# Kernel tuning notes

Hardware: AMD Instinct MI355X
Metric: run time of the kernel (lower is better)

## Reference

```python
import jax, jax.numpy as jnp
import numpy as np

B, DIM, HEADS, Hs, Ws = 8, 192, 8, 128, 128


def setup_inputs() -> dict:
    key = jax.random.key(0)
    ks = jax.random.split(key, 8)
    d3 = 3 * DIM
    inp = {
        "x": jax.random.normal(ks[0], (B, DIM, Hs, Ws), dtype=jnp.float32),
        # qkv 1x1 conv: (out=3*dim, in=dim)
        "w_qkv": jax.random.normal(ks[1], (d3, DIM), dtype=jnp.float32) / np.sqrt(DIM),
        "b_qkv": jnp.zeros((d3,), dtype=jnp.float32),
        # depthwise 3x3 conv, groups = 3*dim -> kernel (3*dim, 1, 3, 3)
        "w_dw": jax.random.normal(ks[2], (d3, 1, 3, 3), dtype=jnp.float32) / 3.0,
        "b_dw": jnp.zeros((d3,), dtype=jnp.float32),
        # project_out 1x1 conv: (dim, dim)
        "w_proj": jax.random.normal(ks[3], (DIM, DIM), dtype=jnp.float32) / np.sqrt(DIM),
        "b_proj": jnp.zeros((DIM,), dtype=jnp.float32),
        "temperature": jnp.ones((HEADS, 1, 1), dtype=jnp.float32),
        "a1": jnp.full((1,), 0.2, dtype=jnp.float32),
        "a2": jnp.full((1,), 0.2, dtype=jnp.float32),
        "a3": jnp.full((1,), 0.2, dtype=jnp.float32),
        "a4": jnp.full((1,), 0.2, dtype=jnp.float32),
    }
    return inp


def _sparse_softmax(attn, k):
    # top-k per row, scatter 1s at those indices, mask rest to -inf, softmax
    _, idx = jax.lax.top_k(attn, k)                      # [..., C, k]
    C = attn.shape[-1]
    mask = jax.nn.one_hot(idx, C, dtype=attn.dtype).sum(-2)  # [..., C, C]
    masked = jnp.where(mask > 0, attn, -jnp.inf)
    return jax.nn.softmax(masked, axis=-1)


def _l2norm(t):
    # torch F.normalize: x / max(||x||_2, eps) along last axis
    n = jnp.sqrt(jnp.sum(t * t, axis=-1, keepdims=True))
    return t / jnp.maximum(n, 1e-12)


def reference(x, w_qkv, b_qkv, w_dw, b_dw, w_proj, b_proj, temperature, a1, a2, a3, a4):
    b, c, h, w = x.shape
    # 1x1 conv
    qkv = jnp.einsum('oi,bihw->bohw', w_qkv, x) + b_qkv[:, None, None]
    # depthwise 3x3 conv, padding=1
    qkv = jax.lax.conv_general_dilated(
        qkv, w_dw, window_strides=(1, 1), padding='SAME',
        feature_group_count=3 * c,
        dimension_numbers=('NCHW', 'OIHW', 'NCHW')) + b_dw[:, None, None]
    q, k, v = jnp.split(qkv, 3, axis=1)
    Cd = c // HEADS  # per-head channel dim
    heads = lambda t: t.reshape(b, HEADS, Cd, h * w)
    q, k, v = heads(q), heads(k), heads(v)
    q, k = _l2norm(q), _l2norm(k)
    # transposed (channel) attention: [b, head, Cd, Cd]
    attn = jnp.einsum('bhcn,bhdn->bhcd', q, k) * temperature
    ks = (int(Cd / 2), int(Cd * 2 / 3), int(Cd * 3 / 4), int(Cd * 4 / 5))
    out1 = jnp.einsum('bhcd,bhdn->bhcn', _sparse_softmax(attn, ks[0]), v)
    out2 = jnp.einsum('bhcd,bhdn->bhcn', _sparse_softmax(attn, ks[1]), v)
    out3 = jnp.einsum('bhcd,bhdn->bhcn', _sparse_softmax(attn, ks[2]), v)
    out4 = jnp.einsum('bhcd,bhdn->bhcn', _sparse_softmax(attn, ks[3]), v)
    out = out1 * a1 + out2 * a2 + out3 * a3 + out4 * a4
    out = out.reshape(b, c, h, w)
    out = jnp.einsum('oi,bihw->bohw', w_proj, out) + b_proj[:, None, None]
    return out
```

## Files before the change

### kernel.cpp

```cpp
#include <hip/hip_runtime.h>
#include <math.h>

#define DIMC 192
#define C3 576
#define NHEADS 8
#define CDh 24
#define HWN 16384
#define WIDTH 128
#define NBATCH 8

typedef __attribute__((ext_vector_type(8))) short short8;
typedef __attribute__((ext_vector_type(4))) float f32x4;

__device__ __forceinline__ ushort f2bf(float f) {
    uint u = __float_as_uint(f);
    u += 0x7fff + ((u >> 16) & 1);
    return (ushort)(u >> 16);
}
__device__ __forceinline__ float bf2f(ushort h) {
    return __uint_as_float(((uint)h) << 16);
}

__global__ void k0_prep(const float* __restrict__ W, ushort* __restrict__ Wh,
                        ushort* __restrict__ Wl, int n) {
    int i = blockIdx.x * 256 + threadIdx.x;
    if (i < n) {
        float w = W[i];
        ushort h = f2bf(w);
        Wh[i] = h;
        Wl[i] = f2bf(w - bf2f(h));
    }
}

__global__ __launch_bounds__(256, 3) void kgx3(const float* __restrict__ x,
                                               const ushort* __restrict__ Wh,
                                               const ushort* __restrict__ Wl,
                                               const float* __restrict__ bias,
                                               float* __restrict__ qkv, long qkv_zs) {
    __shared__ ushort smem[2 * 64 * 200];
    ushort* BsH = smem;
    ushort* BsL = smem + 64 * 200;
    const float* xb = x + (size_t)blockIdx.z * DIMC * HWN;
    float* oz = qkv + (size_t)blockIdx.z * qkv_zs;
    const int n0 = blockIdx.x * 64;
    const int o0 = blockIdx.y * 192;
    const int tid = threadIdx.x;
#pragma unroll
    for (int it = 0; it < 12; it++) {
        int idx = tid + it * 256;
        int ch = idx >> 4, q = idx & 15;
        f32x4 v = *(const f32x4*)&xb[(size_t)ch * HWN + n0 + q * 4];
        const int swz = ((ch >> 3) ^ (q & 7)) * 8 + (ch & 7);
#pragma unroll
        for (int p = 0; p < 4; p++) {
            int ad = (q * 4 + p) * 200 + swz;
            ushort hb = f2bf(v[p]);
            BsH[ad] = hb;
            BsL[ad] = f2bf(v[p] - bf2f(hb));
        }
    }
    __syncthreads();
    const int wid = tid >> 6, lane = tid & 63;
    const int lr = lane & 15, lk = lane >> 4;
    const int mb = o0 + wid * 48;
    f32x4 acc[3][4];
#pragma unroll
    for (int i = 0; i < 3; i++)
#pragma unroll
        for (int j = 0; j < 4; j++) acc[i][j] = (f32x4)0.f;

    for (int kc6 = 0; kc6 < 6; kc6++) {
        short8 bh[4], bl[4];
#pragma unroll
        for (int j = 0; j < 4; j++) {
            int px = j * 16 + lr;
            int o = (kc6 * 4 + lk) ^ ((px >> 2) & 7);
            int ad = px * 200 + o * 8;
            bh[j] = *(const short8*)&BsH[ad];
            bl[j] = *(const short8*)&BsL[ad];
        }
#pragma unroll
        for (int i = 0; i < 3; i++) {
            size_t ao = (size_t)(mb + i * 16 + lr) * DIMC + kc6 * 32 + lk * 8;
            const short8 ah = *(const short8*)&Wh[ao];
            const short8 al = *(const short8*)&Wl[ao];
#pragma unroll
            for (int j = 0; j < 4; j++) {
                acc[i][j] = __builtin_amdgcn_mfma_f32_16x16x32_bf16(ah, bh[j], acc[i][j], 0, 0, 0);
                acc[i][j] = __builtin_amdgcn_mfma_f32_16x16x32_bf16(ah, bl[j], acc[i][j], 0, 0, 0);
                acc[i][j] = __builtin_amdgcn_mfma_f32_16x16x32_bf16(al, bh[j], acc[i][j], 0, 0, 0);
            }
        }
    }
    __syncthreads();
    float* epsb = (float*)smem + wid * (2 * 1056);
#pragma unroll
    for (int i = 0; i < 3; i++) {
        float* eps = epsb + (i & 1) * 1056;
        int rb = mb + i * 16;
#pragma unroll
        for (int j = 0; j < 4; j++)
#pragma unroll
            for (int r = 0; r < 4; r++)
                eps[(lk * 4 + r) * 66 + j * 16 + lr] = acc[i][j][r] + bias[rb + lk * 4 + r];
#pragma unroll
        for (int s = 0; s < 4; s++) {
            int rl = s * 4 + (lane >> 4);
            int c4 = (lane & 15) * 4;
            f32x4 v = *(const f32x4*)&eps[rl * 66 + c4];
            *(f32x4*)&oz[(size_t)(rb + rl) * HWN + n0 + c4] = v;
        }
    }
}

__global__ __launch_bounds__(256, 3) void kg3f(float* __restrict__ vy,
                                               const ushort* __restrict__ Mh,
                                               const ushort* __restrict__ Ml,
                                               const float* __restrict__ bias) {
    __shared__ ushort smem[2 * 64 * 200];
    ushort* BsH = smem;
    ushort* BsL = smem + 64 * 200;
    const int z = blockIdx.y;
    float* vb = vy + (size_t)z * DIMC * HWN;
    const int n0 = blockIdx.x * 64;
    const int tid = threadIdx.x;
#pragma unroll
    for (int it = 0; it < 12; it++) {
        int idx = tid + it * 256;
        int ch = idx >> 4, q = idx & 15;
        f32x4 v = *(const f32x4*)&vb[(size_t)ch * HWN + n0 + q * 4];
        const int swz = ((ch >> 3) ^ (q & 7)) * 8 + (ch & 7);
#pragma unroll
        for (int p = 0; p < 4; p++) {
            int ad = (q * 4 + p) * 200 + swz;
            ushort hb = f2bf(v[p]);
            BsH[ad] = hb;
            BsL[ad] = f2bf(v[p] - bf2f(hb));
        }
    }
    __syncthreads();
    const int wid = tid >> 6, lane = tid & 63;
    const int lr = lane & 15, lk = lane >> 4;
    const int mb = wid * 48;
    const ushort* Azh = Mh + (size_t)z * DIMC * DIMC;
    const ushort* Azl = Ml + (size_t)z * DIMC * DIMC;
    f32x4 acc[3][4];
#pragma unroll
    for (int i = 0; i < 3; i++)
#pragma unroll
        for (int j = 0; j < 4; j++) acc[i][j] = (f32x4)0.f;

    for (int kc6 = 0; kc6 < 6; kc6++) {
        short8 bh[4], bl[4];
#pragma unroll
        for (int j = 0; j < 4; j++) {
            int px = j * 16 + lr;
            int o = (kc6 * 4 + lk) ^ ((px >> 2) & 7);
            int ad = px * 200 + o * 8;
            bh[j] = *(const short8*)&BsH[ad];
            bl[j] = *(const short8*)&BsL[ad];
        }
#pragma unroll
        for (int i = 0; i < 3; i++) {
            size_t ao = (size_t)(mb + i * 16 + lr) * DIMC + kc6 * 32 + lk * 8;
            const short8 ah = *(const short8*)&Azh[ao];
            const short8 al = *(const short8*)&Azl[ao];
#pragma unroll
            for (int j = 0; j < 4; j++) {
                acc[i][j] = __builtin_amdgcn_mfma_f32_16x16x32_bf16(ah, bh[j], acc[i][j], 0, 0, 0);
                acc[i][j] = __builtin_amdgcn_mfma_f32_16x16x32_bf16(ah, bl[j], acc[i][j], 0, 0, 0);
                acc[i][j] = __builtin_amdgcn_mfma_f32_16x16x32_bf16(al, bh[j], acc[i][j], 0, 0, 0);
            }
        }
    }
    __syncthreads();
    float* epsb = (float*)smem + wid * (2 * 1056);
#pragma unroll
    for (int i = 0; i < 3; i++) {
        float* eps = epsb + (i & 1) * 1056;
        int rb = mb + i * 16;
#pragma unroll
        for (int j = 0; j < 4; j++)
#pragma unroll
            for (int r = 0; r < 4; r++)
                eps[(lk * 4 + r) * 66 + j * 16 + lr] = acc[i][j][r] + bias[rb + lk * 4 + r];
#pragma unroll
        for (int s = 0; s < 4; s++) {
            int rl = s * 4 + (lane >> 4);
            int c4 = (lane & 15) * 4;
            f32x4 v = *(const f32x4*)&eps[rl * 66 + c4];
            *(f32x4*)&vb[(size_t)(rb + rl) * HWN + n0 + c4] = v;
        }
    }
}

__global__ __launch_bounds__(1024, 4) void k2_dw(const float* __restrict__ qkv0, long qkv_zs,
                                                 const float* __restrict__ wdw,
                                                 const float* __restrict__ bdw,
                                                 float* __restrict__ vout,
                                                 float* __restrict__ part, int b0) {
    __shared__ float stage[2 * 6336];
    __shared__ float qks[48 * 520];
    const int b = b0 + blockIdx.z;
    const float* qkv = qkv0 + (size_t)blockIdx.z * qkv_zs;
    const int stripe = blockIdx.x, h = blockIdx.y;
    const int tid = threadIdx.x;
    const int r0 = stripe * 4;

    const int col4 = (tid & 31) * 4;
    const int orow = (tid >> 5) & 3;
    const int cc = tid >> 7;

    auto stage_load = [&](int chunk, int buf) {
        const int g = chunk / 3, cb = (chunk % 3) * 8;
        float* sb = stage + buf * 6336;
#pragma unroll
        for (int f = tid; f < 1536; f += 1024) {
            int fc = f / 192, rem = f - fc * 192;
            int rl = rem >> 5, c4 = rem & 31;
            int gr = r0 - 1 + rl;
            int ch = g * DIMC + h * CDh + cb + fc;
            float4 v = make_float4(0.f, 0.f, 0.f, 0.f);
            if (gr >= 0 && gr < 128)
                v = *(const float4*)&qkv[(size_t)ch * HWN + gr * WIDTH + c4 * 4];
            *(float4*)&sb[(fc * 6 + rl) * 132 + c4 * 4] = v;
        }
    };

    stage_load(0, 0);
    __syncthreads();
    for (int chunk = 0; chunk < 9; chunk++) {
        const int buf = chunk & 1;
        if (chunk < 8) stage_load(chunk + 1, buf ^ 1);
        const int g = chunk / 3, cb = (chunk % 3) * 8;
        const float* sb = stage + buf * 6336;
        const int ch = g * DIMC + h * CDh + cb + cc;
        float wr[9];
#pragma unroll
        for (int t = 0; t < 9; t++) wr[t] = wdw[ch * 9 + t];
        float bsv = bdw[ch];
        float a0 = bsv, a1 = bsv, a2 = bsv, a3 = bsv;
#pragma unroll
        for (int dr = 0; dr < 3; dr++) {
            const float* row = &sb[(cc * 6 + orow + dr) * 132];
            f32x4 cen = *(const f32x4*)&row[col4];
            f32x4 lf4 = (col4 > 0) ? *(const f32x4*)&row[col4 - 4] : (f32x4)0.f;
            f32x4 rt4 = (col4 < 124) ? *(const f32x4*)&row[col4 + 4] : (f32x4)0.f;
            float left = lf4[3], right = rt4[0];
            float wA = wr[dr * 3 + 0], wB = wr[dr * 3 + 1], wC = wr[dr * 3 + 2];
            a0 = fmaf(left, wA, fmaf(cen[0], wB, fmaf(cen[1], wC, a0)));
            a1 = fmaf(cen[0], wA, fmaf(cen[1], wB, fmaf(cen[2], wC, a1)));
            a2 = fmaf(cen[1], wA, fmaf(cen[2], wB, fmaf(cen[3], wC, a2)));
            a3 = fmaf(cen[2], wA, fmaf(cen[3], wB, fmaf(right, wC, a3)));
        }
        if (g < 2) {
            float4 o4 = {a0, a1, a2, a3};
            *(float4*)&qks[(g * CDh + cb + cc) * 520 + orow * 128 + col4] = o4;
        } else {
            float4 o4 = {a0, a1, a2, a3};
            *(float4*)&vout[((size_t)b * DIMC + h * CDh + cb + cc) * HWN +
                            (size_t)(r0 + orow) * WIDTH + col4] = o4;
        }
        __syncthreads();
    }

    const int tc = tid & 3, td = (tid >> 2) & 3, tp = tid >> 4;
    float ga[6][6];
#pragma unroll
    for (int i = 0; i < 6; i++)
#pragma unroll
        for (int j = 0; j < 6; j++) ga[i][j] = 0.f;
#pragma unroll
    for (int s = 0; s < 2; s++) {
        int px = tp * 8 + s * 4;
        f32x4 qv[6], kv[6];
#pragma unroll
        for (int i = 0; i < 6; i++) qv[i] = *(const f32x4*)&qks[(tc * 6 + i) * 520 + px];
#pragma unroll
        for (int j = 0; j < 6; j++) kv[j] = *(const f32x4*)&qks[(24 + td * 6 + j) * 520 + px];
#pragma unroll
        for (int i = 0; i < 6; i++)
#pragma unroll
            for (int j = 0; j < 6; j++) {
                ga[i][j] = fmaf(qv[i][0], kv[j][0], ga[i][j]);
                ga[i][j] = fmaf(qv[i][1], kv[j][1], ga[i][j]);
                ga[i][j] = fmaf(qv[i][2], kv[j][2], ga[i][j]);
                ga[i][j] = fmaf(qv[i][3], kv[j][3], ga[i][j]);
            }
    }
#pragma unroll
    for (int i = 0; i < 6; i++)
#pragma unroll
        for (int j = 0; j < 6; j++) {
            float v = ga[i][j];
            v += __shfl_xor(v, 16, 64);
            v += __shfl_xor(v, 32, 64);
            ga[i][j] = v;
        }
    float nv = 0.f;
    int nch = 0, npg = 0;
    if (tid < 768) {
        npg = tid / 48;
        nch = tid - npg * 48;
#pragma unroll
        for (int s = 0; s < 8; s++) {
            f32x4 v = *(const f32x4*)&qks[nch * 520 + npg * 32 + s * 4];
            nv = fmaf(v[0], v[0], nv);
            nv = fmaf(v[1], v[1], nv);
            nv = fmaf(v[2], v[2], nv);
            nv = fmaf(v[3], v[3], nv);
        }
    }
    __syncthreads();
    float* gscr = qks;
    const int wave = tid >> 6;
    if ((tid & 63) < 16) {
#pragma unroll
        for (int i = 0; i < 6; i++)
#pragma unroll
            for (int j = 0; j < 6; j++)
                gscr[wave * 624 + (tc * 6 + i) * 24 + (td * 6 + j)] = ga[i][j];
    }
    if (tid < 768) gscr[npg * 624 + 576 + nch] = nv;
    __syncthreads();
    if (tid < 624) {
        float s = 0.f;
#pragma unroll
        for (int w2 = 0; w2 < 16; w2++) s += gscr[w2 * 624 + tid];
        part[((size_t)(b * NHEADS + h) * 64 + stripe) * 624 + tid] = s;
    }
}

__global__ void k34_attn(const float* __restrict__ part, const float* __restrict__ temp,
                         const float* __restrict__ a1, const float* __restrict__ a2,
                         const float* __restrict__ a3, const float* __restrict__ a4,
                         float* __restrict__ Aeff) {
    __shared__ float gbuf[624];
    int bh = blockIdx.x;
    int h = bh & 7;
    int tid = threadIdx.x;
    for (int ti = tid; ti < 624; ti += 256) {
        float s = 0.f;
        const float* p = part + (size_t)bh * 64 * 624 + ti;
#pragma unroll 4
        for (int st = 0; st < 32; st++) s += p[st * 624];
        gbuf[ti] = s;
    }
    __syncthreads();
    int r = tid;
    if (r >= CDh) return;
    float t = temp[h];
    float aw[4] = {a1[0], a2[0], a3[0], a4[0]};
    const int kks[4] = {12, 16, 18, 19};
    float qn = fmaxf(sqrtf(gbuf[576 + r]), 1e-12f);
    float av[24];
    for (int d = 0; d < 24; d++) {
        float kn = fmaxf(sqrtf(gbuf[600 + d]), 1e-12f);
        av[d] = gbuf[r * 24 + d] / (qn * kn) * t;
    }
    int rank[24];
    float m = -1e30f;
    for (int d = 0; d < 24; d++) {
        int rk = 0;
        for (int e = 0; e < 24; e++)
            rk += (av[e] > av[d]) || (av[e] == av[d] && e < d);
        rank[d] = rk;
        m = fmaxf(m, av[d]);
    }
    float ex[24], outv[24];
    for (int d = 0; d < 24; d++) { ex[d] = expf(av[d] - m); outv[d] = 0.f; }
    for (int i = 0; i < 4; i++) {
        float Z = 0.f;
        for (int d = 0; d < 24; d++) if (rank[d] < kks[i]) Z += ex[d];
        float inv = aw[i] / Z;
        for (int d = 0; d < 24; d++) if (rank[d] < kks[i]) outv[d] += ex[d] * inv;
    }
    for (int d = 0; d < 24; d++) Aeff[(bh * 24 + r) * 24 + d] = outv[d];
}

__global__ void k4b_mmat(const float* __restrict__ Wp, const float* __restrict__ Aeff,
                         ushort* __restrict__ Mh, ushort* __restrict__ Ml) {
    int b = blockIdx.x;
    int e0 = blockIdx.y * 6144;
    for (int e = e0 + threadIdx.x; e < e0 + 6144; e += 256) {
        int o = e / DIMC, j = e % DIMC;
        int h = j / CDh, d = j % CDh;
        const float* wrow = Wp + o * DIMC + h * CDh;
        const float* acol = Aeff + (size_t)((b * NHEADS + h) * CDh) * CDh + d;
        float s = 0.f;
        for (int c = 0; c < CDh; c++) s = fmaf(wrow[c], acol[c * CDh], s);
        size_t idx = ((size_t)b * DIMC + o) * DIMC + j;
        ushort hb = f2bf(s);
        Mh[idx] = hb;
        Ml[idx] = f2bf(s - bf2f(hb));
    }
}

extern "C" void kernel_launch(void* const* d_in, const int* in_sizes, int n_in,
                              void* d_out, int out_size, void* d_ws, size_t ws_size,
                              hipStream_t stream) {
    const float* x     = (const float*)d_in[0];
    const float* wqkv  = (const float*)d_in[1];
    const float* bqkv  = (const float*)d_in[2];
    const float* wdw   = (const float*)d_in[3];
    const float* bdw   = (const float*)d_in[4];
    const float* wproj = (const float*)d_in[5];
    const float* bproj = (const float*)d_in[6];
    const float* temp  = (const float*)d_in[7];
    const float* a1    = (const float*)d_in[8];
    const float* a2    = (const float*)d_in[9];
    const float* a3    = (const float*)d_in[10];
    const float* a4    = (const float*)d_in[11];
    float* out = (float*)d_out;

    float* ws = (float*)d_ws;
    const size_t fl_part = (size_t)64 * 64 * 624;
    const size_t fl_A    = (size_t)64 * 576;
    const size_t fl_M    = (size_t)NBATCH * DIMC * DIMC / 2;
    const size_t fl_W    = (size_t)C3 * DIMC / 2;
    const size_t fl_qkv1 = (size_t)C3 * HWN;
    const size_t base_fl = fl_part + fl_A + 2 * fl_M + 2 * fl_W;

    int nz = (ws_size >= (base_fl + 2 * fl_qkv1) * sizeof(float)) ? 2 : 1;

    size_t o = 0;
    float* part = ws + o; o += fl_part;
    float* Aeff = ws + o; o += fl_A;
    ushort* Mh  = (ushort*)(ws + o); o += fl_M;
    ushort* Ml  = (ushort*)(ws + o); o += fl_M;
    ushort* Wh  = (ushort*)(ws + o); o += fl_W;
    ushort* Wl  = (ushort*)(ws + o); o += fl_W;
    float* qkv  = ws + o;

    const long qkv_zs = (long)fl_qkv1;

    k0_prep<<<(C3 * DIMC + 255) / 256, 256, 0, stream>>>(wqkv, Wh, Wl, C3 * DIMC);

    for (int b0 = 0; b0 < NBATCH; b0 += nz) {
        kgx3<<<dim3(256, 3, nz), 256, 0, stream>>>(x + (size_t)b0 * DIMC * HWN,
                                                   Wh, Wl, bqkv, qkv, qkv_zs);
        k2_dw<<<dim3(32, 8, nz), 1024, 0, stream>>>(qkv, qkv_zs, wdw, bdw, out, part, b0);
    }
    k34_attn<<<64, 256, 0, stream>>>(part, temp, a1, a2, a3, a4, Aeff);
    k4b_mmat<<<dim3(8, 6), 256, 0, stream>>>(wproj, Aeff, Mh, Ml);
    kg3f<<<dim3(256, 8), 256, 0, stream>>>(out, Mh, Ml, bproj);
}
```

Measured before the change: 459.9 us.

## Drop LDS swizzle in GEMM kernels, pad qks stride, raise batch chunking

Measured after the change: 449.5 us. -2.3%, faster.

```diff
diff --git a/kernel.cpp b/kernel.cpp
--- a/kernel.cpp
+++ b/kernel.cpp
@@ -8,6 +8,7 @@
 #define HWN 16384
 #define WIDTH 128
 #define NBATCH 8
+#define QKS 524
 
 typedef __attribute__((ext_vector_type(8))) short short8;
 typedef __attribute__((ext_vector_type(4))) float f32x4;
@@ -50,10 +51,9 @@
         int idx = tid + it * 256;
         int ch = idx >> 4, q = idx & 15;
         f32x4 v = *(const f32x4*)&xb[(size_t)ch * HWN + n0 + q * 4];
-        const int swz = ((ch >> 3) ^ (q & 7)) * 8 + (ch & 7);
 #pragma unroll
         for (int p = 0; p < 4; p++) {
-            int ad = (q * 4 + p) * 200 + swz;
+            int ad = (q * 4 + p) * 200 + ch;
             ushort hb = f2bf(v[p]);
             BsH[ad] = hb;
             BsL[ad] = f2bf(v[p] - bf2f(hb));
@@ -69,13 +69,12 @@
 #pragma unroll
         for (int j = 0; j < 4; j++) acc[i][j] = (f32x4)0.f;
 
+#pragma unroll 2
     for (int kc6 = 0; kc6 < 6; kc6++) {
         short8 bh[4], bl[4];
 #pragma unroll
         for (int j = 0; j < 4; j++) {
-            int px = j * 16 + lr;
-            int o = (kc6 * 4 + lk) ^ ((px >> 2) & 7);
-            int ad = px * 200 + o * 8;
+            int ad = (j * 16 + lr) * 200 + kc6 * 32 + lk * 8;
             bh[j] = *(const short8*)&BsH[ad];
             bl[j] = *(const short8*)&BsL[ad];
         }
@@ -129,10 +128,9 @@
         int idx = tid + it * 256;
         int ch = idx >> 4, q = idx & 15;
         f32x4 v = *(const f32x4*)&vb[(size_t)ch * HWN + n0 + q * 4];
-        const int swz = ((ch >> 3) ^ (q & 7)) * 8 + (ch & 7);
 #pragma unroll
         for (int p = 0; p < 4; p++) {
-            int ad = (q * 4 + p) * 200 + swz;
+            int ad = (q * 4 + p) * 200 + ch;
             ushort hb = f2bf(v[p]);
             BsH[ad] = hb;
             BsL[ad] = f2bf(v[p] - bf2f(hb));
@@ -150,13 +148,12 @@
 #pragma unroll
         for (int j = 0; j < 4; j++) acc[i][j] = (f32x4)0.f;
 
+#pragma unroll 2
     for (int kc6 = 0; kc6 < 6; kc6++) {
         short8 bh[4], bl[4];
 #pragma unroll
         for (int j = 0; j < 4; j++) {
-            int px = j * 16 + lr;
-            int o = (kc6 * 4 + lk) ^ ((px >> 2) & 7);
-            int ad = px * 200 + o * 8;
+            int ad = (j * 16 + lr) * 200 + kc6 * 32 + lk * 8;
             bh[j] = *(const short8*)&BsH[ad];
             bl[j] = *(const short8*)&BsL[ad];
         }
@@ -200,7 +197,7 @@
                                                  float* __restrict__ vout,
                                                  float* __restrict__ part, int b0) {
     __shared__ float stage[2 * 6336];
-    __shared__ float qks[48 * 520];
+    __shared__ float qks[48 * QKS];
     const int b = b0 + blockIdx.z;
     const float* qkv = qkv0 + (size_t)blockIdx.z * qkv_zs;
     const int stripe = blockIdx.x, h = blockIdx.y;
@@ -255,7 +252,7 @@
         }
         if (g < 2) {
             float4 o4 = {a0, a1, a2, a3};
-            *(float4*)&qks[(g * CDh + cb + cc) * 520 + orow * 128 + col4] = o4;
+            *(float4*)&qks[(g * CDh + cb + cc) * QKS + orow * 128 + col4] = o4;
         } else {
             float4 o4 = {a0, a1, a2, a3};
             *(float4*)&vout[((size_t)b * DIMC + h * CDh + cb + cc) * HWN +
@@ -275,9 +272,9 @@
         int px = tp * 8 + s * 4;
         f32x4 qv[6], kv[6];
 #pragma unroll
-        for (int i = 0; i < 6; i++) qv[i] = *(const f32x4*)&qks[(tc * 6 + i) * 520 + px];
-#pragma unroll
-        for (int j = 0; j < 6; j++) kv[j] = *(const f32x4*)&qks[(24 + td * 6 + j) * 520 + px];
+        for (int i = 0; i < 6; i++) qv[i] = *(const f32x4*)&qks[(tc * 6 + i) * QKS + px];
+#pragma unroll
+        for (int j = 0; j < 6; j++) kv[j] = *(const f32x4*)&qks[(24 + td * 6 + j) * QKS + px];
 #pragma unroll
         for (int i = 0; i < 6; i++)
 #pragma unroll
@@ -304,7 +301,7 @@
         nch = tid - npg * 48;
 #pragma unroll
         for (int s = 0; s < 8; s++) {
-            f32x4 v = *(const f32x4*)&qks[nch * 520 + npg * 32 + s * 4];
+            f32x4 v = *(const f32x4*)&qks[nch * QKS + npg * 32 + s * 4];
             nv = fmaf(v[0], v[0], nv);
             nv = fmaf(v[1], v[1], nv);
             nv = fmaf(v[2], v[2], nv);
@@ -421,7 +418,9 @@
     const size_t fl_qkv1 = (size_t)C3 * HWN;
     const size_t base_fl = fl_part + fl_A + 2 * fl_M + 2 * fl_W;
 
-    int nz = (ws_size >= (base_fl + 2 * fl_qkv1) * sizeof(float)) ? 2 : 1;
+    int nz = 1;
+    if (ws_size >= (base_fl + 4 * fl_qkv1) * sizeof(float))      nz = 4;
+    else if (ws_size >= (base_fl + 2 * fl_qkv1) * sizeof(float)) nz = 2;
 
     size_t o = 0;
     float* part = ws + o; o += fl_part;
```
